# Kernel optimization log

Hardware: AMD Instinct MI355X
Metric: run time of the kernel (lower is better)

The kernel has to match this reference:

```python
import jax, jax.numpy as jnp
import numpy as np

LN_EPS = 1e-5  # nn.LayerNorm default
N_HEAD = 12


def layer_norm(x, w, b, eps=LN_EPS):
    m = jnp.mean(x, axis=-1, keepdims=True)
    v = jnp.var(x, axis=-1, keepdims=True)
    return (x - m) * jax.lax.rsqrt(v + eps) * w + b


def mha(x, in_proj_w, in_proj_b, out_w, out_b, n_head):
    # x: [B,S,D]; self-attention, q=k=v=x (torch nn.MultiheadAttention math)
    B, S, D = x.shape
    hd = D // n_head
    qkv = x @ in_proj_w.T + in_proj_b              # [B,S,3D]
    q, k, v = jnp.split(qkv, 3, axis=-1)
    q = q.reshape(B, S, n_head, hd)
    k = k.reshape(B, S, n_head, hd)
    v = v.reshape(B, S, n_head, hd)
    scale = 1.0 / jnp.sqrt(jnp.asarray(hd, x.dtype))
    scores = jnp.einsum('bqhd,bkhd->bhqk', q, k) * scale  # [B,H,S,S]
    attn = jax.nn.softmax(scores, axis=-1)
    o = jnp.einsum('bhqk,bkhd->bqhd', attn, v).reshape(B, S, D)
    return o @ out_w.T + out_b


def setup_inputs() -> dict:
    key = jax.random.key(0)
    ks = jax.random.split(key, 8)
    B, S, D = 4, 2048, 768
    d_ff = 4 * D
    sd = 0.02
    return {
        'x': jax.random.normal(ks[0], (B, S, D), jnp.float32),
        'ln1_w': jnp.ones((D,), jnp.float32),
        'ln1_b': jnp.zeros((D,), jnp.float32),
        'in_proj_w': jax.random.normal(ks[1], (3 * D, D), jnp.float32) * sd,
        'in_proj_b': jax.random.normal(ks[2], (3 * D,), jnp.float32) * sd,
        'out_w': jax.random.normal(ks[3], (D, D), jnp.float32) * sd,
        'out_b': jax.random.normal(ks[4], (D,), jnp.float32) * sd,
        'ln2_w': jnp.ones((D,), jnp.float32),
        'ln2_b': jnp.zeros((D,), jnp.float32),
        'fc_w': jax.random.normal(ks[5], (d_ff, D), jnp.float32) * sd,
        'fc_b': jnp.zeros((d_ff,), jnp.float32),
        'proj_w': jax.random.normal(ks[6], (D, d_ff), jnp.float32) * sd,
        'proj_b': jnp.zeros((D,), jnp.float32),
    }


def reference(x, ln1_w, ln1_b, in_proj_w, in_proj_b, out_w, out_b,
              ln2_w, ln2_b, fc_w, fc_b, proj_w, proj_b):
    h = layer_norm(x, ln1_w, ln1_b)
    x = x + mha(h, in_proj_w, in_proj_b, out_w, out_b, N_HEAD)
    h2 = layer_norm(x, ln2_w, ln2_b)
    mlp = jax.nn.gelu(h2 @ fc_w.T + fc_b, approximate=False) @ proj_w.T + proj_b
    return x + mlp
```

## Files before the change

### kernel.cpp

```cpp
#include <hip/hip_runtime.h>
#include <hip/hip_bf16.h>
#include <math.h>

#define D_MODEL 768
#define N_HEADS 12
#define HD 64
#define SEQ 2048
#define BATCH 4
#define M_ROWS 8192
#define D_FF 3072
#define QKV_DIM 2304
#define LN_EPS 1e-5f

typedef __attribute__((ext_vector_type(8))) short bf16x8;
typedef __attribute__((ext_vector_type(4))) float f32x4;
typedef __hip_bfloat16 bf16;

__device__ __forceinline__ void store_val(float* p, float v) { *p = v; }
__device__ __forceinline__ void store_val(bf16* p, float v) { *p = __float2bfloat16(v); }

__device__ __forceinline__ unsigned int bf16_bits(float v) {
    bf16 b = __float2bfloat16(v);
    unsigned short u;
    __builtin_memcpy(&u, &b, 2);
    return (unsigned int)u;
}

__device__ __forceinline__ void async_load16(const void* g, void* l) {
    __builtin_amdgcn_global_load_lds(
        (const __attribute__((address_space(1))) void*)g,
        (__attribute__((address_space(3))) void*)l, 16, 0, 0);
}

__global__ __launch_bounds__(256) void cast_all(const float* __restrict__ s0, bf16* __restrict__ d0, int n0,
                                                const float* __restrict__ s1, bf16* __restrict__ d1, int n1,
                                                const float* __restrict__ s2, bf16* __restrict__ d2, int n2,
                                                const float* __restrict__ s3, bf16* __restrict__ d3, int n3) {
    int i = blockIdx.x * 256 + threadIdx.x;
    const float* s; bf16* d; int local = i;
    if (local < n0) { s = s0; d = d0; }
    else {
        local -= n0;
        if (local < n1) { s = s1; d = d1; }
        else {
            local -= n1;
            if (local < n2) { s = s2; d = d2; }
            else {
                local -= n2;
                if (local >= n3) return;
                s = s3; d = d3;
            }
        }
    }
    float4 v = ((const float4*)s)[local];
    d[local * 4 + 0] = __float2bfloat16(v.x);
    d[local * 4 + 1] = __float2bfloat16(v.y);
    d[local * 4 + 2] = __float2bfloat16(v.z);
    d[local * 4 + 3] = __float2bfloat16(v.w);
}

template <typename OutT>
__global__ __launch_bounds__(256) void ln_kernel(const float* __restrict__ x,
                                                 const float* __restrict__ w,
                                                 const float* __restrict__ b,
                                                 OutT* __restrict__ y) {
    int row = blockIdx.x;
    const float* xr = x + (size_t)row * D_MODEL;
    OutT* yr = y + (size_t)row * D_MODEL;
    int t = threadIdx.x;
    float v0 = xr[t], v1 = xr[t + 256], v2 = xr[t + 512];
    float s  = v0 + v1 + v2;
    float sq = v0 * v0 + v1 * v1 + v2 * v2;
    #pragma unroll
    for (int off = 32; off; off >>= 1) {
        s  += __shfl_xor(s, off);
        sq += __shfl_xor(sq, off);
    }
    __shared__ float ss[4], ssq[4];
    int wave = t >> 6;
    if ((t & 63) == 0) { ss[wave] = s; ssq[wave] = sq; }
    __syncthreads();
    s  = ss[0] + ss[1] + ss[2] + ss[3];
    sq = ssq[0] + ssq[1] + ssq[2] + ssq[3];
    float mean = s * (1.0f / D_MODEL);
    float var  = sq * (1.0f / D_MODEL) - mean * mean;
    float rstd = rsqrtf(var + LN_EPS);
    store_val(yr + t,       (v0 - mean) * rstd * w[t]       + b[t]);
    store_val(yr + t + 256, (v1 - mean) * rstd * w[t + 256] + b[t + 256]);
    store_val(yr + t + 512, (v2 - mean) * rstd * w[t + 512] + b[t + 512]);
}

__device__ __forceinline__ float gelu_exact(float v) {
    return 0.5f * v * (1.0f + erff(v * 0.70710678118654752f));
}

template <int FUSE, int BNT, typename OutT>
__global__ __launch_bounds__(256) void gemm_mfma(const bf16* __restrict__ A,
                                                 const bf16* __restrict__ W,
                                                 const float* __restrict__ bias,
                                                 const float* __restrict__ resid,
                                                 bf16* __restrict__ vt,
                                                 OutT* __restrict__ C,
                                                 int M, int N, int K) {
    const int BM = 128, BK = 32;
    const int MI = (BNT == 128) ? 4 : 2;
    const int BCH = BNT * 4 / 256;
    __shared__ __align__(16) bf16 As[BM * BK];
    __shared__ __align__(16) bf16 Bs[BNT * BK];
    int t = threadIdx.x;
    int wave = t >> 6, lane = t & 63;
    int m_base = blockIdx.y * BM, n_base = blockIdx.x * BNT;
    int wm = (BNT == 128) ? (wave >> 1) * 64 : wave * 32;
    int wn = (BNT == 128) ? (wave & 1) * 64 : 0;

    f32x4 acc[MI][4] = {};

    const bf16* Ag[2]; const bf16* Bg[2];
    bf16* Al[2]; bf16* Bl[2];
    #pragma unroll
    for (int r = 0; r < 2; r++) {
        int c = r * 256 + t;
        int row = c >> 2, ko = (c & 3) * 8;
        Ag[r] = A + (size_t)(m_base + row) * K + ko;
        Al[r] = As + (r * 256 + wave * 64) * 8;
        if (r < BCH) {
            Bg[r] = W + (size_t)(n_base + row) * K + ko;
            Bl[r] = Bs + (r * 256 + wave * 64) * 8;
        }
    }

    int fr = lane & 15;
    int fk = (lane >> 4) * 8;

    for (int k0 = 0; k0 < K; k0 += BK) {
        __syncthreads();
        #pragma unroll
        for (int r = 0; r < 2; r++) {
            async_load16(Ag[r] + k0, Al[r]);
            if (r < BCH) async_load16(Bg[r] + k0, Bl[r]);
        }
        __syncthreads();

        bf16x8 af[MI], bfr[4];
        #pragma unroll
        for (int mi = 0; mi < MI; mi++)
            af[mi] = *(const bf16x8*)&As[(wm + mi * 16 + fr) * BK + fk];
        #pragma unroll
        for (int ni = 0; ni < 4; ni++)
            bfr[ni] = *(const bf16x8*)&Bs[(wn + ni * 16 + fr) * BK + fk];
        #pragma unroll
        for (int mi = 0; mi < MI; mi++)
            #pragma unroll
            for (int ni = 0; ni < 4; ni++)
                acc[mi][ni] = __builtin_amdgcn_mfma_f32_16x16x32_bf16(
                    af[mi], bfr[ni], acc[mi][ni], 0, 0, 0);
    }

    int rq = (lane >> 4) * 4;
    int c_ = lane & 15;

    if (FUSE == 3 && n_base >= 1536) {
        bf16* T = As;
        int bb = m_base >> 11, s_off = m_base & 2047;
        int d0 = n_base - 1536;
        #pragma unroll
        for (int p = 0; p < 4; p++) {
            __syncthreads();
            if ((wave & 1) == (p >> 1)) {
                int ni0 = (p & 1) * 2;
                #pragma unroll
                for (int q = 0; q < 2; q++) {
                    int nd = ni0 + q;
                    float bv = bias[n_base + wn + nd * 16 + c_];
                    #pragma unroll
                    for (int mi = 0; mi < MI; mi++) {
                        unsigned int lo = bf16_bits(acc[mi][nd][0] + bv) |
                                          (bf16_bits(acc[mi][nd][1] + bv) << 16);
                        unsigned int hi = bf16_bits(acc[mi][nd][2] + bv) |
                                          (bf16_bits(acc[mi][nd][3] + bv) << 16);
                        uint2 pk; pk.x = lo; pk.y = hi;
                        int drel = q * 16 + c_;
                        int s = wm + mi * 16 + rq;
                        *(uint2*)&T[drel * 128 + s] = pk;
                    }
                }
            }
            __syncthreads();
            {
                int r = t >> 3, part = t & 7;
                int d = d0 + p * 32 + r;
                int hh = d >> 6, dd = d & 63;
                bf16* dstp = vt + ((size_t)(bb * N_HEADS + hh) * HD + dd) * SEQ + s_off + part * 16;
                uint4 v0 = *(const uint4*)&T[r * 128 + part * 16];
                uint4 v1 = *(const uint4*)&T[r * 128 + part * 16 + 8];
                *(uint4*)dstp = v0;
                *(uint4*)(dstp + 8) = v1;
            }
        }
        return;
    }

    float scale = (FUSE == 3 && n_base < 768) ? 0.125f : 1.0f;
    #pragma unroll
    for (int mi = 0; mi < MI; mi++) {
        #pragma unroll
        for (int ni = 0; ni < 4; ni++) {
            int col = n_base + wn + ni * 16 + c_;
            float bv = bias[col];
            #pragma unroll
            for (int reg = 0; reg < 4; reg++) {
                int row = m_base + wm + mi * 16 + rq + reg;
                float v = acc[mi][ni][reg] + bv;
                if (FUSE == 1) v = gelu_exact(v);
                if (FUSE == 2) v += resid[(size_t)row * N + col];
                if (FUSE == 3) v *= scale;
                store_val(C + (size_t)row * N + col, v);
            }
        }
    }
}

__global__ __launch_bounds__(256) void attn_mfma(const bf16* __restrict__ qkvb,
                                                 const bf16* __restrict__ vt,
                                                 bf16* __restrict__ o) {
    __shared__ __align__(16) bf16 Qs[2 * 128 * 32];
    __shared__ __align__(16) bf16 Ks[2 * 64 * 32];
    __shared__ __align__(16) bf16 Vts[2 * 64 * 32];
    __shared__ __align__(16) bf16 Ps[128 * 72];

    int t = threadIdx.x;
    int wave = t >> 6, lane = t & 63;
    int qt = blockIdx.x, h = blockIdx.y, b = blockIdx.z;
    int s0 = qt * 128;
    int wq = wave * 32;
    int c = lane & 15, rr = lane >> 4;

    const bf16* qbase  = qkvb + (size_t)b * SEQ * QKV_DIM + h * HD;
    const bf16* kbase  = qbase + D_MODEL;
    const bf16* vtbase = vt + (size_t)((b * N_HEADS + h) * HD) * SEQ;

    #pragma unroll
    for (int r = 0; r < 4; r++) {
        int lin = r * 256 + t;
        int kk = lin >> 9, qq = (lin >> 2) & 127, qo = lin & 3;
        async_load16(qbase + (size_t)(s0 + qq) * QKV_DIM + kk * 32 + qo * 8,
                     Qs + (size_t)(r * 256 + wave * 64) * 8);
    }
    __syncthreads();

    bf16x8 aq[2][2];
    #pragma unroll
    for (int m = 0; m < 2; m++)
        #pragma unroll
        for (int kk = 0; kk < 2; kk++)
            aq[m][kk] = *(const bf16x8*)&Qs[kk * 4096 + (wq + m * 16 + c) * 32 + rr * 8];

    f32x4 Oa[2][4] = {};
    float l_part[2][4] = {};

    for (int jt = 0; jt < SEQ; jt += 64) {
        __syncthreads();
        #pragma unroll
        for (int r = 0; r < 2; r++) {
            int lin = r * 256 + t;
            int kk = lin >> 8, jj = (lin >> 2) & 63, qo = lin & 3;
            async_load16(kbase + (size_t)(jt + jj) * QKV_DIM + kk * 32 + qo * 8,
                         Ks + (size_t)(r * 256 + wave * 64) * 8);
            async_load16(vtbase + (size_t)jj * SEQ + jt + kk * 32 + qo * 8,
                         Vts + (size_t)(r * 256 + wave * 64) * 8);
        }
        __syncthreads();

        f32x4 S[2][4] = {};
        #pragma unroll
        for (int kk = 0; kk < 2; kk++) {
            bf16x8 bk[4];
            #pragma unroll
            for (int n = 0; n < 4; n++)
                bk[n] = *(const bf16x8*)&Ks[kk * 2048 + (n * 16 + c) * 32 + rr * 8];
            #pragma unroll
            for (int n = 0; n < 4; n++)
                #pragma unroll
                for (int m = 0; m < 2; m++)
                    S[m][n] = __builtin_amdgcn_mfma_f32_16x16x32_bf16(
                        aq[m][kk], bk[n], S[m][n], 0, 0, 0);
        }

        #pragma unroll
        for (int m = 0; m < 2; m++) {
            #pragma unroll
            for (int rg = 0; rg < 4; rg++) {
                int qrow = wq + m * 16 + rr * 4 + rg;
                float psum = 0.0f;
                #pragma unroll
                for (int n = 0; n < 4; n++) {
                    float p = __expf(S[m][n][rg]);
                    psum += p;
                    Ps[qrow * 72 + n * 16 + c] = __float2bfloat16(p);
                }
                l_part[m][rg] += psum;
            }
        }

        #pragma unroll
        for (int kk = 0; kk < 2; kk++) {
            bf16x8 ap[2];
            #pragma unroll
            for (int m = 0; m < 2; m++)
                ap[m] = *(const bf16x8*)&Ps[(wq + m * 16 + c) * 72 + kk * 32 + rr * 8];
            #pragma unroll
            for (int n = 0; n < 4; n++) {
                bf16x8 bv = *(const bf16x8*)&Vts[kk * 2048 + (n * 16 + c) * 32 + rr * 8];
                #pragma unroll
                for (int m = 0; m < 2; m++)
                    Oa[m][n] = __builtin_amdgcn_mfma_f32_16x16x32_bf16(
                        ap[m], bv, Oa[m][n], 0, 0, 0);
            }
        }
    }

    #pragma unroll
    for (int m = 0; m < 2; m++)
        #pragma unroll
        for (int rg = 0; rg < 4; rg++) {
            float l = l_part[m][rg];
            #pragma unroll
            for (int off = 8; off; off >>= 1) l += __shfl_xor(l, off);
            float inv = 1.0f / l;
            int q = s0 + wq + m * 16 + rr * 4 + rg;
            bf16* op = o + (size_t)(b * SEQ + q) * D_MODEL + h * HD;
            #pragma unroll
            for (int n = 0; n < 4; n++)
                op[n * 16 + c] = __float2bfloat16(Oa[m][n][rg] * inv);
        }
}

extern "C" void kernel_launch(void* const* d_in, const int* in_sizes, int n_in,
                              void* d_out, int out_size, void* d_ws, size_t ws_size,
                              hipStream_t stream) {
    const float* x         = (const float*)d_in[0];
    const float* ln1_w     = (const float*)d_in[1];
    const float* ln1_b     = (const float*)d_in[2];
    const float* in_proj_w = (const float*)d_in[3];
    const float* in_proj_b = (const float*)d_in[4];
    const float* out_w     = (const float*)d_in[5];
    const float* out_b     = (const float*)d_in[6];
    const float* ln2_w     = (const float*)d_in[7];
    const float* ln2_b     = (const float*)d_in[8];
    const float* fc_w      = (const float*)d_in[9];
    const float* fc_b      = (const float*)d_in[10];
    const float* proj_w    = (const float*)d_in[11];
    const float* proj_b    = (const float*)d_in[12];

    float* out = (float*)d_out;
    char*  ws  = (char*)d_ws;

    bf16* qkvb = (bf16*)ws;
    bf16* vt   = (bf16*)(ws + 37748736);
    bf16* ff   = (bf16*)ws;
    bf16* h    = (bf16*)(ws + 50331648);
    bf16* o    = (bf16*)(ws + 62914560);
    bf16* wbf  = (bf16*)(ws + 75497472);
    bf16* wqkv_b  = wbf;
    bf16* wout_b  = wqkv_b + (size_t)QKV_DIM * D_MODEL;
    bf16* wfc_b   = wout_b + (size_t)D_MODEL * D_MODEL;
    bf16* wproj_b = wfc_b  + (size_t)D_FF * D_MODEL;

    {
        int n0 = QKV_DIM * D_MODEL / 4, n1 = D_MODEL * D_MODEL / 4;
        int n2 = D_FF * D_MODEL / 4,    n3 = D_MODEL * D_FF / 4;
        int tot = n0 + n1 + n2 + n3;
        cast_all<<<(tot + 255) / 256, 256, 0, stream>>>(
            in_proj_w, wqkv_b, n0, out_w, wout_b, n1, fc_w, wfc_b, n2, proj_w, wproj_b, n3);
    }

    ln_kernel<bf16><<<M_ROWS, 256, 0, stream>>>(x, ln1_w, ln1_b, h);
    gemm_mfma<3, 128, bf16><<<dim3(QKV_DIM / 128, M_ROWS / 128), 256, 0, stream>>>(
        h, wqkv_b, in_proj_b, nullptr, vt, qkvb, M_ROWS, QKV_DIM, D_MODEL);
    attn_mfma<<<dim3(SEQ / 128, N_HEADS, BATCH), 256, 0, stream>>>(qkvb, vt, o);
    gemm_mfma<2, 64, float><<<dim3(D_MODEL / 64, M_ROWS / 128), 256, 0, stream>>>(
        o, wout_b, out_b, x, nullptr, out, M_ROWS, D_MODEL, D_MODEL);
    ln_kernel<bf16><<<M_ROWS, 256, 0, stream>>>(out, ln2_w, ln2_b, h);
    gemm_mfma<1, 128, bf16><<<dim3(D_FF / 128, M_ROWS / 128), 256, 0, stream>>>(
        h, wfc_b, fc_b, nullptr, nullptr, ff, M_ROWS, D_FF, D_MODEL);
    gemm_mfma<2, 64, float><<<dim3(D_MODEL / 64, M_ROWS / 128), 256, 0, stream>>>(
        ff, wproj_b, proj_b, out, nullptr, out, M_ROWS, D_MODEL, D_FF);
}
```

Baseline: 441.9 us.

## Fuse LN1 with weight cast, fold log2e into Q scale, transpose score MFMA

The weight-cast kernel and the first LayerNorm are merged into a single launch, with extra blocks handling the casts, which removes one kernel launch and its serialization. The Q scale now includes log2(e), so the softmax can use the native exp2 instruction instead of __expf. The score MFMA is computed transposed (K as the A operand), which lets each lane pack four probabilities into a single 8-byte LDS store and keep one row-sum accumulator per m. This reduces exp work, LDS store count and shuffle reductions, at the cost of a different lane-to-row mapping and a final shuffle to broadcast the row sums.

```diff
diff --git a/kernel.cpp b/kernel.cpp
--- a/kernel.cpp
+++ b/kernel.cpp
@@ -11,6 +11,7 @@
 #define D_FF 3072
 #define QKV_DIM 2304
 #define LN_EPS 1e-5f
+#define Q_SCALE 0.18033688011112042f
 
 typedef __attribute__((ext_vector_type(8))) short bf16x8;
 typedef __attribute__((ext_vector_type(4))) float f32x4;
@@ -32,31 +33,61 @@
         (__attribute__((address_space(3))) void*)l, 16, 0, 0);
 }
 
-__global__ __launch_bounds__(256) void cast_all(const float* __restrict__ s0, bf16* __restrict__ d0, int n0,
-                                                const float* __restrict__ s1, bf16* __restrict__ d1, int n1,
-                                                const float* __restrict__ s2, bf16* __restrict__ d2, int n2,
-                                                const float* __restrict__ s3, bf16* __restrict__ d3, int n3) {
-    int i = blockIdx.x * 256 + threadIdx.x;
-    const float* s; bf16* d; int local = i;
-    if (local < n0) { s = s0; d = d0; }
-    else {
-        local -= n0;
-        if (local < n1) { s = s1; d = d1; }
+__global__ __launch_bounds__(256) void ln1_cast(
+        const float* __restrict__ x, const float* __restrict__ w,
+        const float* __restrict__ b, bf16* __restrict__ y,
+        const float* __restrict__ s0, bf16* __restrict__ d0, int n0,
+        const float* __restrict__ s1, bf16* __restrict__ d1, int n1,
+        const float* __restrict__ s2, bf16* __restrict__ d2, int n2,
+        const float* __restrict__ s3, bf16* __restrict__ d3, int n3) {
+    int t = threadIdx.x;
+    if (blockIdx.x >= M_ROWS) {
+        int i = (blockIdx.x - M_ROWS) * 256 + t;
+        const float* s; bf16* d; int local = i;
+        if (local < n0) { s = s0; d = d0; }
         else {
-            local -= n1;
-            if (local < n2) { s = s2; d = d2; }
+            local -= n0;
+            if (local < n1) { s = s1; d = d1; }
             else {
-                local -= n2;
-                if (local >= n3) return;
-                s = s3; d = d3;
-            }
-        }
-    }
-    float4 v = ((const float4*)s)[local];
-    d[local * 4 + 0] = __float2bfloat16(v.x);
-    d[local * 4 + 1] = __float2bfloat16(v.y);
-    d[local * 4 + 2] = __float2bfloat16(v.z);
-    d[local * 4 + 3] = __float2bfloat16(v.w);
+                local -= n1;
+                if (local < n2) { s = s2; d = d2; }
+                else {
+                    local -= n2;
+                    if (local >= n3) return;
+                    s = s3; d = d3;
+                }
+            }
+        }
+        float4 v = ((const float4*)s)[local];
+        d[local * 4 + 0] = __float2bfloat16(v.x);
+        d[local * 4 + 1] = __float2bfloat16(v.y);
+        d[local * 4 + 2] = __float2bfloat16(v.z);
+        d[local * 4 + 3] = __float2bfloat16(v.w);
+        return;
+    }
+    int row = blockIdx.x;
+    const float* xr = x + (size_t)row * D_MODEL;
+    bf16* yr = y + (size_t)row * D_MODEL;
+    float v0 = xr[t], v1 = xr[t + 256], v2 = xr[t + 512];
+    float s  = v0 + v1 + v2;
+    float sq = v0 * v0 + v1 * v1 + v2 * v2;
+    #pragma unroll
+    for (int off = 32; off; off >>= 1) {
+        s  += __shfl_xor(s, off);
+        sq += __shfl_xor(sq, off);
+    }
+    __shared__ float ss[4], ssq[4];
+    int wave = t >> 6;
+    if ((t & 63) == 0) { ss[wave] = s; ssq[wave] = sq; }
+    __syncthreads();
+    s  = ss[0] + ss[1] + ss[2] + ss[3];
+    sq = ssq[0] + ssq[1] + ssq[2] + ssq[3];
+    float mean = s * (1.0f / D_MODEL);
+    float var  = sq * (1.0f / D_MODEL) - mean * mean;
+    float rstd = rsqrtf(var + LN_EPS);
+    yr[t]       = __float2bfloat16((v0 - mean) * rstd * w[t]       + b[t]);
+    yr[t + 256] = __float2bfloat16((v1 - mean) * rstd * w[t + 256] + b[t + 256]);
+    yr[t + 512] = __float2bfloat16((v2 - mean) * rstd * w[t + 512] + b[t + 512]);
 }
 
 template <typename OutT>
@@ -200,7 +231,7 @@
         return;
     }
 
-    float scale = (FUSE == 3 && n_base < 768) ? 0.125f : 1.0f;
+    float scale = (FUSE == 3 && n_base < 768) ? Q_SCALE : 1.0f;
     #pragma unroll
     for (int mi = 0; mi < MI; mi++) {
         #pragma unroll
@@ -248,15 +279,15 @@
     }
     __syncthreads();
 
-    bf16x8 aq[2][2];
+    bf16x8 bq[2][2];
     #pragma unroll
     for (int m = 0; m < 2; m++)
         #pragma unroll
         for (int kk = 0; kk < 2; kk++)
-            aq[m][kk] = *(const bf16x8*)&Qs[kk * 4096 + (wq + m * 16 + c) * 32 + rr * 8];
+            bq[m][kk] = *(const bf16x8*)&Qs[kk * 4096 + (wq + m * 16 + c) * 32 + rr * 8];
 
     f32x4 Oa[2][4] = {};
-    float l_part[2][4] = {};
+    float l_part[2] = {};
 
     for (int jt = 0; jt < SEQ; jt += 64) {
         __syncthreads();
@@ -271,34 +302,34 @@
         }
         __syncthreads();
 
-        f32x4 S[2][4] = {};
+        f32x4 St[4][2] = {};
         #pragma unroll
         for (int kk = 0; kk < 2; kk++) {
-            bf16x8 bk[4];
-            #pragma unroll
-            for (int n = 0; n < 4; n++)
-                bk[n] = *(const bf16x8*)&Ks[kk * 2048 + (n * 16 + c) * 32 + rr * 8];
-            #pragma unroll
-            for (int n = 0; n < 4; n++)
+            bf16x8 ak[4];
+            #pragma unroll
+            for (int jj = 0; jj < 4; jj++)
+                ak[jj] = *(const bf16x8*)&Ks[kk * 2048 + (jj * 16 + c) * 32 + rr * 8];
+            #pragma unroll
+            for (int jj = 0; jj < 4; jj++)
                 #pragma unroll
                 for (int m = 0; m < 2; m++)
-                    S[m][n] = __builtin_amdgcn_mfma_f32_16x16x32_bf16(
-                        aq[m][kk], bk[n], S[m][n], 0, 0, 0);
-        }
-
-        #pragma unroll
-        for (int m = 0; m < 2; m++) {
-            #pragma unroll
-            for (int rg = 0; rg < 4; rg++) {
-                int qrow = wq + m * 16 + rr * 4 + rg;
-                float psum = 0.0f;
-                #pragma unroll
-                for (int n = 0; n < 4; n++) {
-                    float p = __expf(S[m][n][rg]);
-                    psum += p;
-                    Ps[qrow * 72 + n * 16 + c] = __float2bfloat16(p);
-                }
-                l_part[m][rg] += psum;
+                    St[jj][m] = __builtin_amdgcn_mfma_f32_16x16x32_bf16(
+                        ak[jj], bq[m][kk], St[jj][m], 0, 0, 0);
+        }
+
+        #pragma unroll
+        for (int jj = 0; jj < 4; jj++) {
+            #pragma unroll
+            for (int m = 0; m < 2; m++) {
+                float p0 = __builtin_amdgcn_exp2f(St[jj][m][0]);
+                float p1 = __builtin_amdgcn_exp2f(St[jj][m][1]);
+                float p2 = __builtin_amdgcn_exp2f(St[jj][m][2]);
+                float p3 = __builtin_amdgcn_exp2f(St[jj][m][3]);
+                l_part[m] += (p0 + p1) + (p2 + p3);
+                uint2 pk;
+                pk.x = bf16_bits(p0) | (bf16_bits(p1) << 16);
+                pk.y = bf16_bits(p2) | (bf16_bits(p3) << 16);
+                *(uint2*)&Ps[(wq + m * 16 + c) * 72 + jj * 16 + rr * 4] = pk;
             }
         }
 
@@ -319,14 +350,19 @@
         }
     }
 
+    float lred[2];
+    #pragma unroll
+    for (int m = 0; m < 2; m++) {
+        float l = l_part[m];
+        l += __shfl_xor(l, 16);
+        l += __shfl_xor(l, 32);
+        lred[m] = l;
+    }
     #pragma unroll
     for (int m = 0; m < 2; m++)
         #pragma unroll
         for (int rg = 0; rg < 4; rg++) {
-            float l = l_part[m][rg];
-            #pragma unroll
-            for (int off = 8; off; off >>= 1) l += __shfl_xor(l, off);
-            float inv = 1.0f / l;
+            float inv = 1.0f / __shfl(lred[m], rr * 4 + rg);
             int q = s0 + wq + m * 16 + rr * 4 + rg;
             bf16* op = o + (size_t)(b * SEQ + q) * D_MODEL + h * HD;
             #pragma unroll
@@ -366,15 +402,13 @@
     bf16* wfc_b   = wout_b + (size_t)D_MODEL * D_MODEL;
     bf16* wproj_b = wfc_b  + (size_t)D_FF * D_MODEL;
 
-    {
-        int n0 = QKV_DIM * D_MODEL / 4, n1 = D_MODEL * D_MODEL / 4;
-        int n2 = D_FF * D_MODEL / 4,    n3 = D_MODEL * D_FF / 4;
-        int tot = n0 + n1 + n2 + n3;
-        cast_all<<<(tot + 255) / 256, 256, 0, stream>>>(
-            in_proj_w, wqkv_b, n0, out_w, wout_b, n1, fc_w, wfc_b, n2, proj_w, wproj_b, n3);
-    }
-
-    ln_kernel<bf16><<<M_ROWS, 256, 0, stream>>>(x, ln1_w, ln1_b, h);
+    int n0 = QKV_DIM * D_MODEL / 4, n1 = D_MODEL * D_MODEL / 4;
+    int n2 = D_FF * D_MODEL / 4,    n3 = D_MODEL * D_FF / 4;
+    int cast_blocks = (n0 + n1 + n2 + n3 + 255) / 256;
+
+    ln1_cast<<<M_ROWS + cast_blocks, 256, 0, stream>>>(
+        x, ln1_w, ln1_b, h,
+        in_proj_w, wqkv_b, n0, out_w, wout_b, n1, fc_w, wfc_b, n2, proj_w, wproj_b, n3);
     gemm_mfma<3, 128, bf16><<<dim3(QKV_DIM / 128, M_ROWS / 128), 256, 0, stream>>>(
         h, wqkv_b, in_proj_b, nullptr, vt, qkvb, M_ROWS, QKV_DIM, D_MODEL);
     attn_mfma<<<dim3(SEQ / 128, N_HEADS, BATCH), 256, 0, stream>>>(qkvb, vt, o);
```

New measurement: 441.0 us. About the same (-0.2%).
